# Performance work log

Hardware: AMD Instinct MI355X
Metric: run time of the kernel (lower is better)

## Reference

```python
import jax, jax.numpy as jnp
import numpy as np

D_HEAD = 64
D_MODEL = 1024
N_HEADS = D_MODEL // D_HEAD
MAX_TOKENS = 2048


def setup_inputs() -> dict:
    key = jax.random.key(0)
    ks = jax.random.split(key, 5)
    batch, pos = 2, 2048
    # kaiming_normal_ on (n_heads, d_model, d_head): fan_in = d_model*d_head -> std = sqrt(2/fan_in)
    std_qkv = np.sqrt(2.0 / (D_MODEL * D_HEAD)).astype(np.float32)
    # xavier_normal_ on (d_model, d_model): std = sqrt(2/(fan_in+fan_out))
    std_out = np.sqrt(2.0 / (D_MODEL + D_MODEL)).astype(np.float32)
    return {
        "residual_stream": jax.random.normal(ks[0], (batch, pos, D_MODEL), dtype=jnp.float32),
        "weight_query": jax.random.normal(ks[1], (N_HEADS, D_MODEL, D_HEAD), dtype=jnp.float32) * std_qkv,
        "weight_key": jax.random.normal(ks[2], (N_HEADS, D_MODEL, D_HEAD), dtype=jnp.float32) * std_qkv,
        "weight_value": jax.random.normal(ks[3], (N_HEADS, D_MODEL, D_HEAD), dtype=jnp.float32) * std_qkv,
        "weight_out": jax.random.normal(ks[4], (D_MODEL, D_MODEL), dtype=jnp.float32) * std_out,
    }


def reference(residual_stream, weight_query, weight_key, weight_value, weight_out):
    # QKV projections: [b, p, m] x [h, m, d] -> [b, h, p, d]
    q = jnp.einsum('bpm,hmd->bhpd', residual_stream, weight_query)
    k = jnp.einsum('bpm,hmd->bhpd', residual_stream, weight_key)
    v = jnp.einsum('bpm,hmd->bhpd', residual_stream, weight_value)

    n_tokens = residual_stream.shape[1]
    # scaled scores [b, h, dest, src]
    scores = jnp.einsum('bhqd,bhkd->bhqk', q, k) / jnp.sqrt(jnp.float32(D_HEAD))
    # causal mask: -inf above the diagonal
    causal = jnp.tril(jnp.ones((n_tokens, n_tokens), dtype=bool))
    scores = jnp.where(causal, scores, jnp.float32(-jnp.inf))
    pattern = jax.nn.softmax(scores, axis=-1)

    attn = jnp.einsum('bhqk,bhkd->bhqd', pattern, v)  # [b, h, dest, d_head]
    # concat heads -> [b, p, h*d_head]
    b, h, p, d = attn.shape
    attn_concat = jnp.transpose(attn, (0, 2, 1, 3)).reshape(b, p, h * d)
    return jnp.einsum('bpm,mn->bpn', attn_concat, weight_out)
```

## Files before the change

kernel.cpp:

```cpp
#include <hip/hip_runtime.h>
#include <hip/hip_bf16.h>
#include <stdint.h>


typedef __bf16 bf16x8 __attribute__((ext_vector_type(8)));
typedef float f32x4 __attribute__((ext_vector_type(4)));
typedef unsigned short u16;

__device__ __forceinline__ u16 f2bf(float f) {
  unsigned u = __float_as_uint(f);
  u += 0x7fffu + ((u >> 16) & 1u);
  return (u16)(u >> 16);
}

__global__ __launch_bounds__(256) void xcvt_k(const float* __restrict__ in,
                                              u16* __restrict__ out) {
  int i = (blockIdx.x * 256 + threadIdx.x) * 8;
  float4 f0 = *reinterpret_cast<const float4*>(in + i);
  float4 f1 = *reinterpret_cast<const float4*>(in + i + 4);
  u16 tmp[8] = {f2bf(f0.x), f2bf(f0.y), f2bf(f0.z), f2bf(f0.w),
                f2bf(f1.x), f2bf(f1.y), f2bf(f1.z), f2bf(f1.w)};
  *reinterpret_cast<uint4*>(out + i) = *reinterpret_cast<uint4*>(tmp);
}

__global__ __launch_bounds__(256) void transpose_cvt_k(const float* __restrict__ in,
                                                       u16* __restrict__ out,
                                                       int R, int C) {
  __shared__ u16 tile[64][80];
  int b = blockIdx.z;
  int r0 = blockIdx.x * 64, c0 = blockIdx.y * 64;
  const float* ip = in + (size_t)b * R * C;
  u16* op = out + (size_t)b * R * C;
  int t = threadIdx.x;
  int r = t >> 2, cb = (t & 3) * 16;
  const float4* src = reinterpret_cast<const float4*>(ip + (size_t)(r0 + r) * C + c0 + cb);
  u16 tmp[16];
#pragma unroll
  for (int v = 0; v < 4; v++) {
    float4 f = src[v];
    tmp[v * 4 + 0] = f2bf(f.x);
    tmp[v * 4 + 1] = f2bf(f.y);
    tmp[v * 4 + 2] = f2bf(f.z);
    tmp[v * 4 + 3] = f2bf(f.w);
  }
  *reinterpret_cast<uint4*>(&tile[r][cb]) = *reinterpret_cast<uint4*>(&tmp[0]);
  *reinterpret_cast<uint4*>(&tile[r][cb + 8]) = *reinterpret_cast<uint4*>(&tmp[8]);
  __syncthreads();
  int c = t >> 2, rb = (t & 3) * 16;
  uint4 outv[2];
  u16* tp = reinterpret_cast<u16*>(outv);
#pragma unroll
  for (int j = 0; j < 16; j++) tp[j] = tile[rb + j][c];
  uint4* dst = reinterpret_cast<uint4*>(op + (size_t)(c0 + c) * R + r0 + rb);
  dst[0] = outv[0];
  dst[1] = outv[1];
}

__global__ __launch_bounds__(256) void transpose_qkv_k(const float* __restrict__ Wq,
                                                       const float* __restrict__ Wk,
                                                       const float* __restrict__ Wv,
                                                       u16* __restrict__ outBase) {
  __shared__ u16 tile[64][80];
  int z = blockIdx.z;
  int sel = z >> 4, head = z & 15;
  const float* W = (sel == 0) ? Wq : (sel == 1 ? Wk : Wv);
  const float* ip = W + (size_t)head * 65536;
  u16* op = outBase + (size_t)sel * 1048576 + (size_t)head * 65536;
  int r0 = blockIdx.x * 64;
  int t = threadIdx.x;
  int r = t >> 2, cb = (t & 3) * 16;
  const float4* src = reinterpret_cast<const float4*>(ip + (size_t)(r0 + r) * 64 + cb);
  u16 tmp[16];
#pragma unroll
  for (int v = 0; v < 4; v++) {
    float4 f = src[v];
    tmp[v * 4 + 0] = f2bf(f.x);
    tmp[v * 4 + 1] = f2bf(f.y);
    tmp[v * 4 + 2] = f2bf(f.z);
    tmp[v * 4 + 3] = f2bf(f.w);
  }
  *reinterpret_cast<uint4*>(&tile[r][cb]) = *reinterpret_cast<uint4*>(&tmp[0]);
  *reinterpret_cast<uint4*>(&tile[r][cb + 8]) = *reinterpret_cast<uint4*>(&tmp[8]);
  __syncthreads();
  int c = t >> 2, rb = (t & 3) * 16;
  uint4 outv[2];
  u16* tp = reinterpret_cast<u16*>(outv);
#pragma unroll
  for (int j = 0; j < 16; j++) tp[j] = tile[rb + j][c];
  uint4* dst = reinterpret_cast<uint4*>(op + (size_t)c * 1024 + r0 + rb);
  dst[0] = outv[0];
  dst[1] = outv[1];
}

__device__ __forceinline__ void gload16(const u16* g, u16* l) {
  __builtin_amdgcn_global_load_lds(
      (__attribute__((address_space(1))) void*)(g),
      (__attribute__((address_space(3))) void*)(l), 16, 0, 0);
}

__device__ __forceinline__ void gemm128_core(const u16* __restrict__ A,
                                             const u16* __restrict__ BT,
                                             int m0, int n0,
                                             f32x4 (&acc)[4][4]) {
  __shared__ __align__(16) u16 As[128][64];
  __shared__ __align__(16) u16 Bs[128][64];
  int t = threadIdx.x, l = t & 63;
  int w = t >> 6, wm = w & 1, wn = w >> 1;
  int l15 = l & 15, q4 = l >> 4;
  int srow = w * 32 + (l >> 3);
  int scol = (l & 7) * 8;
  const u16* ga = A + (size_t)(m0 + srow) * 1024 + scol;
  const u16* gb = BT + (size_t)(n0 + srow) * 1024 + scol;
  f32x4 z4 = {0.f, 0.f, 0.f, 0.f};
#pragma unroll
  for (int mi = 0; mi < 4; mi++)
#pragma unroll
    for (int nt = 0; nt < 4; nt++) acc[mi][nt] = z4;

  for (int k0 = 0; k0 < 1024; k0 += 64) {
    __syncthreads();
#pragma unroll
    for (int i = 0; i < 4; i++) {
      gload16(ga + (size_t)(i * 8) * 1024 + k0, &As[w * 32 + i * 8][0]);
      gload16(gb + (size_t)(i * 8) * 1024 + k0, &Bs[w * 32 + i * 8][0]);
    }
    __syncthreads();
#pragma unroll
    for (int kk = 0; kk < 2; kk++) {
      bf16x8 af[4], bfr[4];
#pragma unroll
      for (int mi = 0; mi < 4; mi++)
        af[mi] = *reinterpret_cast<const bf16x8*>(&As[wm * 64 + mi * 16 + l15][kk * 32 + q4 * 8]);
#pragma unroll
      for (int nt = 0; nt < 4; nt++)
        bfr[nt] = *reinterpret_cast<const bf16x8*>(&Bs[wn * 64 + nt * 16 + l15][kk * 32 + q4 * 8]);
#pragma unroll
      for (int mi = 0; mi < 4; mi++)
#pragma unroll
        for (int nt = 0; nt < 4; nt++)
          acc[mi][nt] = __builtin_amdgcn_mfma_f32_16x16x32_bf16(af[mi], bfr[nt], acc[mi][nt], 0, 0, 0);
    }
  }
}

__global__ __launch_bounds__(256) void qkv_gemm128_k(const u16* __restrict__ A,
                                                     const u16* __restrict__ BT,
                                                     u16* __restrict__ Q,
                                                     u16* __restrict__ K,
                                                     u16* __restrict__ VT2) {
  const float QSCALE = 0.125f * 1.44269504088896340736f;
  int m0 = blockIdx.x * 128, n0 = blockIdx.y * 128;
  f32x4 acc[4][4];
  gemm128_core(A, BT, m0, n0, acc);
  int t = threadIdx.x, l = t & 63;
  int w = t >> 6, wm = w & 1, wn = w >> 1;
  int l15 = l & 15, q4 = l >> 4;
#pragma unroll
  for (int mi = 0; mi < 4; mi++) {
#pragma unroll
    for (int nt = 0; nt < 4; nt++) {
#pragma unroll
      for (int r = 0; r < 4; r++) {
        int m = m0 + wm * 64 + mi * 16 + q4 * 4 + r;
        int n = n0 + wn * 64 + nt * 16 + l15;
        int wsel = n >> 10, h = (n >> 6) & 15, d = n & 63;
        int b = m >> 11, p = m & 2047;
        size_t bh = (size_t)(b * 16 + h);
        float v = acc[mi][nt][r];
        if (wsel == 0)
          Q[(bh * 2048 + p) * 64 + d] = f2bf(v * QSCALE);
        else if (wsel == 1)
          K[(bh * 2048 + p) * 64 + d] = f2bf(v);
        else
          VT2[((bh * 32 + (p >> 6)) * 64 + d) * 64 + (p & 63)] = f2bf(v);
      }
    }
  }
}

__global__ __launch_bounds__(256) void out_gemm128_k(const u16* __restrict__ A,
                                                     const u16* __restrict__ BT,
                                                     float* __restrict__ O) {
  int m0 = blockIdx.x * 128, n0 = blockIdx.y * 128;
  f32x4 acc[4][4];
  gemm128_core(A, BT, m0, n0, acc);
  int t = threadIdx.x, l = t & 63;
  int w = t >> 6, wm = w & 1, wn = w >> 1;
  int l15 = l & 15, q4 = l >> 4;
#pragma unroll
  for (int mi = 0; mi < 4; mi++) {
#pragma unroll
    for (int nt = 0; nt < 4; nt++) {
#pragma unroll
      for (int r = 0; r < 4; r++) {
        int m = m0 + wm * 64 + mi * 16 + q4 * 4 + r;
        int n = n0 + wn * 64 + nt * 16 + l15;
        O[(size_t)m * 1024 + n] = acc[mi][nt][r];
      }
    }
  }
}

__global__ __launch_bounds__(256) void attn_k(const u16* __restrict__ Q,
                                              const u16* __restrict__ K,
                                              const u16* __restrict__ VT2,
                                              u16* __restrict__ A) {
  __shared__ u16 Ks[2][64][72];
  __shared__ u16 Vs[2][64][72];
  __shared__ u16 P[4][32][80];
  int pr = blockIdx.x, h = blockIdx.y, b = blockIdx.z;
  size_t bh = (size_t)(b * 16 + h);
  const u16* Qp = Q + bh * 2048 * 64;
  const u16* Kp = K + bh * 2048 * 64;
  const u16* Vt = VT2 + bh * 32 * 64 * 64;
  int t = threadIdx.x, l = t & 63, w = t >> 6;
  int l15 = l & 15, q4 = l >> 4;
  const float NEG = -1e30f;
  f32x4 z4 = {0.f, 0.f, 0.f, 0.f};
  int srow = (t & 127) >> 1, shalf = t & 1;
  bool isV = t >= 128;
  const u16* sbase = (isV ? Vt : Kp) + (size_t)srow * 64 + shalf * 32;

#pragma unroll
  for (int which = 0; which < 2; which++) {
    int qt = which ? (15 - pr) : pr;
    int nkt = 2 * qt + 2;
    int qr0 = qt * 128 + w * 32;
    bf16x8 qf[2][2];
#pragma unroll
    for (int mi = 0; mi < 2; mi++) {
      const u16* qp = Qp + (size_t)(qr0 + mi * 16 + l15) * 64;
      qf[mi][0] = *reinterpret_cast<const bf16x8*>(qp + q4 * 8);
      qf[mi][1] = *reinterpret_cast<const bf16x8*>(qp + 32 + q4 * 8);
    }
    f32x4 accO[2][4];
    float rs[2][4];
#pragma unroll
    for (int mi = 0; mi < 2; mi++) {
#pragma unroll
      for (int nt = 0; nt < 4; nt++) accO[mi][nt] = z4;
#pragma unroll
      for (int r = 0; r < 4; r++) rs[mi][r] = 0.f;
    }

    {
      const uint4* s4 = reinterpret_cast<const uint4*>(sbase);
      uint4 v0 = s4[0], v1 = s4[1], v2 = s4[2], v3 = s4[3];
      uint4* d4 = isV ? reinterpret_cast<uint4*>(&Vs[0][srow][shalf * 32])
                      : reinterpret_cast<uint4*>(&Ks[0][srow][shalf * 32]);
      d4[0] = v0; d4[1] = v1; d4[2] = v2; d4[3] = v3;
    }
    __syncthreads();

    for (int kt = 0; kt < nkt; kt++) {
      int cur = kt & 1;
      bool more = kt < nkt - 1;
      uint4 n0, n1, n2, n3;
      if (more) {
        const uint4* s4 = reinterpret_cast<const uint4*>(sbase + (size_t)(kt + 1) * 4096);
        n0 = s4[0]; n1 = s4[1]; n2 = s4[2]; n3 = s4[3];
      }

      f32x4 s[2][4];
#pragma unroll
      for (int mi = 0; mi < 2; mi++)
#pragma unroll
        for (int nt = 0; nt < 4; nt++) s[mi][nt] = z4;
      __builtin_amdgcn_s_setprio(1);
#pragma unroll
      for (int kk = 0; kk < 2; kk++) {
        bf16x8 kf[4];
#pragma unroll
        for (int nt = 0; nt < 4; nt++)
          kf[nt] = *reinterpret_cast<const bf16x8*>(&Ks[cur][nt * 16 + l15][kk * 32 + q4 * 8]);
#pragma unroll
        for (int mi = 0; mi < 2; mi++)
#pragma unroll
          for (int nt = 0; nt < 4; nt++)
            s[mi][nt] = __builtin_amdgcn_mfma_f32_16x16x32_bf16(qf[mi][kk], kf[nt], s[mi][nt], 0, 0, 0);
      }
      __builtin_amdgcn_s_setprio(0);
      if (kt >= 2 * qt) {
        int colbase = (kt - 2 * qt) * 64;
        int rowl = w * 32 + q4 * 4;
#pragma unroll
        for (int mi = 0; mi < 2; mi++)
#pragma unroll
          for (int nt = 0; nt < 4; nt++)
#pragma unroll
            for (int r = 0; r < 4; r++)
              if (colbase + nt * 16 + l15 > rowl + mi * 16 + r) s[mi][nt][r] = NEG;
      }
#pragma unroll
      for (int mi = 0; mi < 2; mi++)
#pragma unroll
        for (int nt = 0; nt < 4; nt++)
#pragma unroll
          for (int r = 0; r < 4; r++) {
            float p = exp2f(s[mi][nt][r]);
            rs[mi][r] += p;
            P[w][mi * 16 + q4 * 4 + r][nt * 16 + l15] = f2bf(p);
          }
      __builtin_amdgcn_s_setprio(1);
#pragma unroll
      for (int kk = 0; kk < 2; kk++) {
        bf16x8 pa[2];
#pragma unroll
        for (int mi = 0; mi < 2; mi++)
          pa[mi] = *reinterpret_cast<const bf16x8*>(&P[w][mi * 16 + l15][kk * 32 + q4 * 8]);
#pragma unroll
        for (int nt = 0; nt < 4; nt++) {
          bf16x8 vf = *reinterpret_cast<const bf16x8*>(&Vs[cur][nt * 16 + l15][kk * 32 + q4 * 8]);
#pragma unroll
          for (int mi = 0; mi < 2; mi++)
            accO[mi][nt] = __builtin_amdgcn_mfma_f32_16x16x32_bf16(pa[mi], vf, accO[mi][nt], 0, 0, 0);
        }
      }
      __builtin_amdgcn_s_setprio(0);

      if (more) {
        uint4* d4 = isV ? reinterpret_cast<uint4*>(&Vs[cur ^ 1][srow][shalf * 32])
                        : reinterpret_cast<uint4*>(&Ks[cur ^ 1][srow][shalf * 32]);
        d4[0] = n0; d4[1] = n1; d4[2] = n2; d4[3] = n3;
      }
      __syncthreads();
    }
#pragma unroll
    for (int mi = 0; mi < 2; mi++)
#pragma unroll
      for (int r = 0; r < 4; r++) {
        float v = rs[mi][r];
#pragma unroll
        for (int sh = 1; sh < 16; sh <<= 1) v += __shfl_xor(v, sh, 64);
        float inv = 1.f / v;
        int prow = qt * 128 + w * 32 + mi * 16 + q4 * 4 + r;
        size_t base = ((size_t)(b * 2048 + prow)) * 1024 + h * 64;
#pragma unroll
        for (int nt = 0; nt < 4; nt++) A[base + nt * 16 + l15] = f2bf(accO[mi][nt][r] * inv);
      }
  }
}

extern "C" void kernel_launch(void* const* d_in, const int* in_sizes, int n_in,
                              void* d_out, int out_size, void* d_ws, size_t ws_size,
                              hipStream_t stream) {
  const float* X  = (const float*)d_in[0];
  const float* Wq = (const float*)d_in[1];
  const float* Wk = (const float*)d_in[2];
  const float* Wv = (const float*)d_in[3];
  const float* Wo = (const float*)d_in[4];
  float* out = (float*)d_out;

  u16* ws = (u16*)d_ws;
  u16* WqT = ws;
  u16* WoT = WqT + 3145728;
  u16* Xb  = WoT + 1048576;
  u16* Qb  = Xb + 4194304;
  u16* Kb  = Qb + 4194304;
  u16* VT2 = Kb + 4194304;
  u16* Ab  = Xb;

  xcvt_k<<<dim3(2048), 256, 0, stream>>>(X, Xb);
  transpose_qkv_k<<<dim3(16, 1, 48), 256, 0, stream>>>(Wq, Wk, Wv, WqT);
  transpose_cvt_k<<<dim3(16, 16, 1), 256, 0, stream>>>(Wo, WoT, 1024, 1024);

  qkv_gemm128_k<<<dim3(32, 24), 256, 0, stream>>>(Xb, WqT, Qb, Kb, VT2);
  attn_k<<<dim3(8, 16, 2), 256, 0, stream>>>(Qb, Kb, VT2, Ab);
  out_gemm128_k<<<dim3(32, 8), 256, 0, stream>>>(Ab, WoT, out);
}
```

Measured before the change: 227.0 us.

## Swizzle LDS tiles, use direct global-to-LDS loads, split attention per q-tile

Replaces padded LDS tiles in the GEMM core and the attention kernel with unpadded 64-wide tiles using an XOR chunk swizzle to avoid bank conflicts. The attention kernel now streams K/V tiles with global_load_lds instead of staging through registers. It also launches one block per query tile (twice as many blocks) instead of pairing tiles pr and 15-pr in a single block. The aim is to cut LDS footprint, register pressure and bank conflicts and to raise parallelism. The cost is that per-block causal work becomes unbalanced, since pairing no longer evens it out.

```diff
diff --git a/kernel.cpp b/kernel.cpp
--- a/kernel.cpp
+++ b/kernel.cpp
@@ -107,10 +107,12 @@
   int t = threadIdx.x, l = t & 63;
   int w = t >> 6, wm = w & 1, wn = w >> 1;
   int l15 = l & 15, q4 = l >> 4;
-  int srow = w * 32 + (l >> 3);
-  int scol = (l & 7) * 8;
-  const u16* ga = A + (size_t)(m0 + srow) * 1024 + scol;
-  const u16* gb = BT + (size_t)(n0 + srow) * 1024 + scol;
+  int r8 = l >> 3;
+  int cs = ((l & 7) ^ r8) * 8;
+  int swz = l15 & 7;
+  int srow = w * 32 + r8;
+  const u16* ga = A + (size_t)(m0 + srow) * 1024 + cs;
+  const u16* gb = BT + (size_t)(n0 + srow) * 1024 + cs;
   f32x4 z4 = {0.f, 0.f, 0.f, 0.f};
 #pragma unroll
   for (int mi = 0; mi < 4; mi++)
@@ -130,10 +132,12 @@
       bf16x8 af[4], bfr[4];
 #pragma unroll
       for (int mi = 0; mi < 4; mi++)
-        af[mi] = *reinterpret_cast<const bf16x8*>(&As[wm * 64 + mi * 16 + l15][kk * 32 + q4 * 8]);
+        af[mi] = *reinterpret_cast<const bf16x8*>(
+            &As[wm * 64 + mi * 16 + l15][((kk * 4 + q4) ^ swz) * 8]);
 #pragma unroll
       for (int nt = 0; nt < 4; nt++)
-        bfr[nt] = *reinterpret_cast<const bf16x8*>(&Bs[wn * 64 + nt * 16 + l15][kk * 32 + q4 * 8]);
+        bfr[nt] = *reinterpret_cast<const bf16x8*>(
+            &Bs[wn * 64 + nt * 16 + l15][((kk * 4 + q4) ^ swz) * 8]);
 #pragma unroll
       for (int mi = 0; mi < 4; mi++)
 #pragma unroll
@@ -205,140 +209,135 @@
                                               const u16* __restrict__ K,
                                               const u16* __restrict__ VT2,
                                               u16* __restrict__ A) {
-  __shared__ u16 Ks[2][64][72];
-  __shared__ u16 Vs[2][64][72];
-  __shared__ u16 P[4][32][80];
+  __shared__ __align__(16) u16 Ks[2][64][64];
+  __shared__ __align__(16) u16 Vs[2][64][64];
+  __shared__ u16 P[4][32][72];
   int pr = blockIdx.x, h = blockIdx.y, b = blockIdx.z;
+  int qt = b ? (15 - pr) : pr;
   size_t bh = (size_t)(b * 16 + h);
   const u16* Qp = Q + bh * 2048 * 64;
   const u16* Kp = K + bh * 2048 * 64;
   const u16* Vt = VT2 + bh * 32 * 64 * 64;
   int t = threadIdx.x, l = t & 63, w = t >> 6;
   int l15 = l & 15, q4 = l >> 4;
+  int r8 = l >> 3, cs = ((l & 7) ^ r8) * 8;
+  int swz = l15 & 7;
   const float NEG = -1e30f;
   f32x4 z4 = {0.f, 0.f, 0.f, 0.f};
-  int srow = (t & 127) >> 1, shalf = t & 1;
-  bool isV = t >= 128;
-  const u16* sbase = (isV ? Vt : Kp) + (size_t)srow * 64 + shalf * 32;
-
-#pragma unroll
-  for (int which = 0; which < 2; which++) {
-    int qt = which ? (15 - pr) : pr;
-    int nkt = 2 * qt + 2;
-    int qr0 = qt * 128 + w * 32;
-    bf16x8 qf[2][2];
-#pragma unroll
-    for (int mi = 0; mi < 2; mi++) {
-      const u16* qp = Qp + (size_t)(qr0 + mi * 16 + l15) * 64;
-      qf[mi][0] = *reinterpret_cast<const bf16x8*>(qp + q4 * 8);
-      qf[mi][1] = *reinterpret_cast<const bf16x8*>(qp + 32 + q4 * 8);
-    }
-    f32x4 accO[2][4];
-    float rs[2][4];
-#pragma unroll
-    for (int mi = 0; mi < 2; mi++) {
-#pragma unroll
-      for (int nt = 0; nt < 4; nt++) accO[mi][nt] = z4;
-#pragma unroll
-      for (int r = 0; r < 4; r++) rs[mi][r] = 0.f;
-    }
-
-    {
-      const uint4* s4 = reinterpret_cast<const uint4*>(sbase);
-      uint4 v0 = s4[0], v1 = s4[1], v2 = s4[2], v3 = s4[3];
-      uint4* d4 = isV ? reinterpret_cast<uint4*>(&Vs[0][srow][shalf * 32])
-                      : reinterpret_cast<uint4*>(&Ks[0][srow][shalf * 32]);
-      d4[0] = v0; d4[1] = v1; d4[2] = v2; d4[3] = v3;
-    }
+  int nkt = 2 * qt + 2;
+  const u16* kbase = Kp + (size_t)(w * 16 + r8) * 64 + cs;
+  const u16* vbase = Vt + (size_t)(w * 16 + r8) * 64 + cs;
+
+  int qr0 = qt * 128 + w * 32;
+  bf16x8 qf[2][2];
+#pragma unroll
+  for (int mi = 0; mi < 2; mi++) {
+    const u16* qp = Qp + (size_t)(qr0 + mi * 16 + l15) * 64;
+    qf[mi][0] = *reinterpret_cast<const bf16x8*>(qp + q4 * 8);
+    qf[mi][1] = *reinterpret_cast<const bf16x8*>(qp + 32 + q4 * 8);
+  }
+  f32x4 accO[2][4];
+  float rs[2][4];
+#pragma unroll
+  for (int mi = 0; mi < 2; mi++) {
+#pragma unroll
+    for (int nt = 0; nt < 4; nt++) accO[mi][nt] = z4;
+#pragma unroll
+    for (int r = 0; r < 4; r++) rs[mi][r] = 0.f;
+  }
+
+#pragma unroll
+  for (int j = 0; j < 2; j++) {
+    gload16(kbase + (size_t)(j * 512), &Ks[0][w * 16 + j * 8][0]);
+    gload16(vbase + (size_t)(j * 512), &Vs[0][w * 16 + j * 8][0]);
+  }
+  __syncthreads();
+
+  for (int kt = 0; kt < nkt; kt++) {
+    int cur = kt & 1;
+    if (kt < nkt - 1) {
+      size_t off = (size_t)(kt + 1) * 4096;
+#pragma unroll
+      for (int j = 0; j < 2; j++) {
+        gload16(kbase + off + j * 512, &Ks[cur ^ 1][w * 16 + j * 8][0]);
+        gload16(vbase + off + j * 512, &Vs[cur ^ 1][w * 16 + j * 8][0]);
+      }
+    }
+
+    f32x4 s[2][4];
+#pragma unroll
+    for (int mi = 0; mi < 2; mi++)
+#pragma unroll
+      for (int nt = 0; nt < 4; nt++) s[mi][nt] = z4;
+    __builtin_amdgcn_s_setprio(1);
+#pragma unroll
+    for (int kk = 0; kk < 2; kk++) {
+      bf16x8 kf[4];
+#pragma unroll
+      for (int nt = 0; nt < 4; nt++)
+        kf[nt] = *reinterpret_cast<const bf16x8*>(
+            &Ks[cur][nt * 16 + l15][((kk * 4 + q4) ^ swz) * 8]);
+#pragma unroll
+      for (int mi = 0; mi < 2; mi++)
+#pragma unroll
+        for (int nt = 0; nt < 4; nt++)
+          s[mi][nt] = __builtin_amdgcn_mfma_f32_16x16x32_bf16(qf[mi][kk], kf[nt], s[mi][nt], 0, 0, 0);
+    }
+    __builtin_amdgcn_s_setprio(0);
+    if (kt >= 2 * qt) {
+      int colbase = (kt - 2 * qt) * 64;
+      int rowl = w * 32 + q4 * 4;
+#pragma unroll
+      for (int mi = 0; mi < 2; mi++)
+#pragma unroll
+        for (int nt = 0; nt < 4; nt++)
+#pragma unroll
+          for (int r = 0; r < 4; r++)
+            if (colbase + nt * 16 + l15 > rowl + mi * 16 + r) s[mi][nt][r] = NEG;
+    }
+#pragma unroll
+    for (int mi = 0; mi < 2; mi++)
+#pragma unroll
+      for (int nt = 0; nt < 4; nt++)
+#pragma unroll
+        for (int r = 0; r < 4; r++) {
+          float p = exp2f(s[mi][nt][r]);
+          rs[mi][r] += p;
+          P[w][mi * 16 + q4 * 4 + r][nt * 16 + l15] = f2bf(p);
+        }
+    __builtin_amdgcn_s_setprio(1);
+#pragma unroll
+    for (int kk = 0; kk < 2; kk++) {
+      bf16x8 pa[2];
+#pragma unroll
+      for (int mi = 0; mi < 2; mi++)
+        pa[mi] = *reinterpret_cast<const bf16x8*>(&P[w][mi * 16 + l15][kk * 32 + q4 * 8]);
+#pragma unroll
+      for (int nt = 0; nt < 4; nt++) {
+        bf16x8 vf = *reinterpret_cast<const bf16x8*>(
+            &Vs[cur][nt * 16 + l15][((kk * 4 + q4) ^ swz) * 8]);
+#pragma unroll
+        for (int mi = 0; mi < 2; mi++)
+          accO[mi][nt] = __builtin_amdgcn_mfma_f32_16x16x32_bf16(pa[mi], vf, accO[mi][nt], 0, 0, 0);
+      }
+    }
+    __builtin_amdgcn_s_setprio(0);
     __syncthreads();
-
-    for (int kt = 0; kt < nkt; kt++) {
-      int cur = kt & 1;
-      bool more = kt < nkt - 1;
-      uint4 n0, n1, n2, n3;
-      if (more) {
-        const uint4* s4 = reinterpret_cast<const uint4*>(sbase + (size_t)(kt + 1) * 4096);
-        n0 = s4[0]; n1 = s4[1]; n2 = s4[2]; n3 = s4[3];
-      }
-
-      f32x4 s[2][4];
-#pragma unroll
-      for (int mi = 0; mi < 2; mi++)
-#pragma unroll
-        for (int nt = 0; nt < 4; nt++) s[mi][nt] = z4;
-      __builtin_amdgcn_s_setprio(1);
-#pragma unroll
-      for (int kk = 0; kk < 2; kk++) {
-        bf16x8 kf[4];
-#pragma unroll
-        for (int nt = 0; nt < 4; nt++)
-          kf[nt] = *reinterpret_cast<const bf16x8*>(&Ks[cur][nt * 16 + l15][kk * 32 + q4 * 8]);
-#pragma unroll
-        for (int mi = 0; mi < 2; mi++)
-#pragma unroll
-          for (int nt = 0; nt < 4; nt++)
-            s[mi][nt] = __builtin_amdgcn_mfma_f32_16x16x32_bf16(qf[mi][kk], kf[nt], s[mi][nt], 0, 0, 0);
-      }
-      __builtin_amdgcn_s_setprio(0);
-      if (kt >= 2 * qt) {
-        int colbase = (kt - 2 * qt) * 64;
-        int rowl = w * 32 + q4 * 4;
-#pragma unroll
-        for (int mi = 0; mi < 2; mi++)
-#pragma unroll
-          for (int nt = 0; nt < 4; nt++)
-#pragma unroll
-            for (int r = 0; r < 4; r++)
-              if (colbase + nt * 16 + l15 > rowl + mi * 16 + r) s[mi][nt][r] = NEG;
-      }
-#pragma unroll
-      for (int mi = 0; mi < 2; mi++)
-#pragma unroll
-        for (int nt = 0; nt < 4; nt++)
-#pragma unroll
-          for (int r = 0; r < 4; r++) {
-            float p = exp2f(s[mi][nt][r]);
-            rs[mi][r] += p;
-            P[w][mi * 16 + q4 * 4 + r][nt * 16 + l15] = f2bf(p);
-          }
-      __builtin_amdgcn_s_setprio(1);
-#pragma unroll
-      for (int kk = 0; kk < 2; kk++) {
-        bf16x8 pa[2];
-#pragma unroll
-        for (int mi = 0; mi < 2; mi++)
-          pa[mi] = *reinterpret_cast<const bf16x8*>(&P[w][mi * 16 + l15][kk * 32 + q4 * 8]);
-#pragma unroll
-        for (int nt = 0; nt < 4; nt++) {
-          bf16x8 vf = *reinterpret_cast<const bf16x8*>(&Vs[cur][nt * 16 + l15][kk * 32 + q4 * 8]);
-#pragma unroll
-          for (int mi = 0; mi < 2; mi++)
-            accO[mi][nt] = __builtin_amdgcn_mfma_f32_16x16x32_bf16(pa[mi], vf, accO[mi][nt], 0, 0, 0);
-        }
-      }
-      __builtin_amdgcn_s_setprio(0);
-
-      if (more) {
-        uint4* d4 = isV ? reinterpret_cast<uint4*>(&Vs[cur ^ 1][srow][shalf * 32])
-                        : reinterpret_cast<uint4*>(&Ks[cur ^ 1][srow][shalf * 32]);
-        d4[0] = n0; d4[1] = n1; d4[2] = n2; d4[3] = n3;
-      }
-      __syncthreads();
-    }
-#pragma unroll
-    for (int mi = 0; mi < 2; mi++)
-#pragma unroll
-      for (int r = 0; r < 4; r++) {
-        float v = rs[mi][r];
-#pragma unroll
-        for (int sh = 1; sh < 16; sh <<= 1) v += __shfl_xor(v, sh, 64);
-        float inv = 1.f / v;
-        int prow = qt * 128 + w * 32 + mi * 16 + q4 * 4 + r;
-        size_t base = ((size_t)(b * 2048 + prow)) * 1024 + h * 64;
-#pragma unroll
-        for (int nt = 0; nt < 4; nt++) A[base + nt * 16 + l15] = f2bf(accO[mi][nt][r] * inv);
-      }
-  }
+  }
+
+#pragma unroll
+  for (int mi = 0; mi < 2; mi++)
+#pragma unroll
+    for (int r = 0; r < 4; r++) {
+      float v = rs[mi][r];
+#pragma unroll
+      for (int sh = 1; sh < 16; sh <<= 1) v += __shfl_xor(v, sh, 64);
+      float inv = 1.f / v;
+      int prow = qt * 128 + w * 32 + mi * 16 + q4 * 4 + r;
+      size_t base = ((size_t)(b * 2048 + prow)) * 1024 + h * 64;
+#pragma unroll
+      for (int nt = 0; nt < 4; nt++) A[base + nt * 16 + l15] = f2bf(accO[mi][nt][r] * inv);
+    }
 }
 
 extern "C" void kernel_launch(void* const* d_in, const int* in_sizes, int n_in,
@@ -365,6 +364,6 @@
   transpose_cvt_k<<<dim3(16, 16, 1), 256, 0, stream>>>(Wo, WoT, 1024, 1024);
 
   qkv_gemm128_k<<<dim3(32, 24), 256, 0, stream>>>(Xb, WqT, Qb, Kb, VT2);
-  attn_k<<<dim3(8, 16, 2), 256, 0, stream>>>(Qb, Kb, VT2, Ab);
+  attn_k<<<dim3(16, 16, 2), 256, 0, stream>>>(Qb, Kb, VT2, Ab);
   out_gemm128_k<<<dim3(32, 8), 256, 0, stream>>>(Ab, WoT, out);
 }
```

After: 210.7 us. 1.08x faster.
